# Performance work log

Measured on AMD Instinct MI355X. Metric: run time of the kernel, lower is better.

The kernel has to match this reference:

```python
import jax, jax.numpy as jnp
import numpy as np
import math

B, N, L = 1, 256, 384
D_MSA, D_PAIR, H, DH = 256, 128, 8, 32
EPS = 1e-5


def layernorm(x, g, b):
    mu = jnp.mean(x, axis=-1, keepdims=True)
    var = jnp.mean(jnp.square(x - mu), axis=-1, keepdims=True)
    return (x - mu) * jax.lax.rsqrt(var + EPS) * g + b


def setup_inputs() -> dict:
    key = jax.random.key(0)
    ks = jax.random.split(key, 16)
    s_msa = 1.0 / math.sqrt(D_MSA)
    s_pair = 1.0 / math.sqrt(D_PAIR)
    s_hd = 1.0 / math.sqrt(H * DH)
    return {
        "msa": jax.random.normal(ks[0], (B, N, L, D_MSA), jnp.float32),
        "pair": jax.random.normal(ks[1], (B, L, L, D_PAIR), jnp.float32),
        "ln_msa_g": jnp.ones((D_MSA,), jnp.float32),
        "ln_msa_b": jnp.zeros((D_MSA,), jnp.float32),
        "ln_pair_g": jnp.ones((D_PAIR,), jnp.float32),
        "ln_pair_b": jnp.zeros((D_PAIR,), jnp.float32),
        # SequenceWeight projections (stored as (in, out): y = x @ W + b)
        "Wq_sw": jax.random.normal(ks[2], (D_MSA, H * DH), jnp.float32) * s_msa,
        "bq_sw": jnp.zeros((H * DH,), jnp.float32),
        "Wk_sw": jax.random.normal(ks[3], (D_MSA, H * DH), jnp.float32) * s_msa,
        "bk_sw": jnp.zeros((H * DH,), jnp.float32),
        # Main attention projections (bias-free q/k/v)
        "Wq": jax.random.normal(ks[4], (D_MSA, H * DH), jnp.float32) * s_msa,
        "Wk": jax.random.normal(ks[5], (D_MSA, H * DH), jnp.float32) * s_msa,
        "Wv": jax.random.normal(ks[6], (D_MSA, H * DH), jnp.float32) * s_msa,
        "Wb": jax.random.normal(ks[7], (D_PAIR, H), jnp.float32) * s_pair,
        "Wg": jax.random.normal(ks[8], (D_MSA, H * DH), jnp.float32) * s_msa,
        "bg": jnp.ones((H * DH,), jnp.float32),
        "Wo": jax.random.normal(ks[9], (H * DH, D_MSA), jnp.float32) * s_hd,
        "bo": jnp.zeros((D_MSA,), jnp.float32),
    }


def reference(msa, pair, ln_msa_g, ln_msa_b, ln_pair_g, ln_pair_b,
              Wq_sw, bq_sw, Wk_sw, bk_sw, Wq, Wk, Wv, Wb, Wg, bg, Wo, bo):
    b, n, l, _ = msa.shape
    scale = 1.0 / math.sqrt(DH)

    m = layernorm(msa, ln_msa_g, ln_msa_b)  # (B,N,L,d_msa)

    # --- SequenceWeight: per-sequence, per-position, per-head weights ---
    q_sw = (m[:, 0] @ Wq_sw + bq_sw).reshape(b, l, H, DH) * scale   # (B,L,h,d)
    k_sw = (m @ Wk_sw + bk_sw).reshape(b, n, l, H, DH)              # (B,N,L,h,d)
    sw_logits = jnp.einsum('bihd,bnihd->bnih', q_sw, k_sw)
    seq_weight = jax.nn.softmax(sw_logits, axis=1)[..., None]       # (B,N,L,h,1)

    # --- Row attention with pair bias ---
    q = (m @ Wq).reshape(b, n, l, H, DH) * seq_weight               # seq-weighted queries
    k = (m @ Wk).reshape(b, n, l, H, DH) * scale
    logits = jnp.einsum('bnihd,bnjhd->bijh', q, k)                  # sum over N and d
    bias = layernorm(pair, ln_pair_g, ln_pair_b) @ Wb               # (B,L,L,h)
    attn = jax.nn.softmax(logits + bias, axis=2)                    # softmax over j

    v = (m @ Wv).reshape(b, n, l, H, DH)
    out = jnp.einsum('bijh,bnjhd->bnihd', attn, v).reshape(b, n, l, H * DH)

    gate = jax.nn.sigmoid(m @ Wg + bg)
    return (out * gate) @ Wo + bo                                   # (B,N,L,d_msa)
```

## Files before the change

kernel.cpp:

```cpp
#include <hip/hip_runtime.h>
#include <stdint.h>

#define NSEQ 256
#define LRES 384
#define NH   8
#define NL   (NSEQ*LRES)
#define SCALE 0.17677669529663687f

typedef unsigned short u16;
typedef unsigned int   u32;
typedef short bf16x8 __attribute__((ext_vector_type(8)));
typedef float f32x4  __attribute__((ext_vector_type(4)));

__device__ __forceinline__ u16 f2bf(float f) {
    u32 x = __float_as_uint(f);
    return (u16)((x + 0x7fffu + ((x >> 16) & 1u)) >> 16);
}
__device__ __forceinline__ u32 pack2(float a, float b) {
    u32 xa = __float_as_uint(a);
    u32 xb = __float_as_uint(b);
    xa = (xa + 0x7fffu + ((xa >> 16) & 1u)) >> 16;
    xb = ((xb + 0x7fffu + ((xb >> 16) & 1u)) >> 16) << 16;
    return xa | xb;
}
__device__ __forceinline__ uint4 pack8(const float f[8]) {
    uint4 r;
    r.x = pack2(f[0], f[1]); r.y = pack2(f[2], f[3]);
    r.z = pack2(f[4], f[5]); r.w = pack2(f[6], f[7]);
    return r;
}
__device__ __forceinline__ void unpack2(u32 u, float& f0, float& f1) {
    f0 = __uint_as_float((u & 0xffffu) << 16);
    f1 = __uint_as_float(u & 0xffff0000u);
}
__device__ __forceinline__ void unpack8(uint4 p, float f[8]) {
    unpack2(p.x, f[0], f[1]);
    unpack2(p.y, f[2], f[3]);
    unpack2(p.z, f[4], f[5]);
    unpack2(p.w, f[6], f[7]);
}

__device__ __forceinline__ float wred_sum(float v) {
#pragma unroll
    for (int o = 32; o > 0; o >>= 1) v += __shfl_xor(v, o, 64);
    return v;
}
__device__ __forceinline__ float wred_max(float v) {
#pragma unroll
    for (int o = 32; o > 0; o >>= 1) v = fmaxf(v, __shfl_xor(v, o, 64));
    return v;
}

__global__ __launch_bounds__(256) void ln_msa_k(
    const float* __restrict__ x, const float* __restrict__ g,
    const float* __restrict__ b, u16* __restrict__ lnA,
    float* __restrict__ stats)
{
    const int lane = threadIdx.x & 63;
    const int row = blockIdx.x * 4 + (threadIdx.x >> 6);
    const size_t base = (size_t)row * 256 + lane * 4;
    float4 v = *(const float4*)(x + base);
    float s  = wred_sum(v.x + v.y + v.z + v.w);
    float sq = wred_sum(v.x*v.x + v.y*v.y + v.z*v.z + v.w*v.w);
    const float mu  = s * (1.f / 256.f);
    const float var = sq * (1.f / 256.f) - mu * mu;
    const float rs  = rsqrtf(var + 1e-5f);
    if (lane == 0) {
        stats[(size_t)row * 2]     = mu;
        stats[(size_t)row * 2 + 1] = rs;
    }
    float4 gg = *(const float4*)(g + lane * 4);
    float4 bb = *(const float4*)(b + lane * 4);
    float f0 = (v.x - mu) * rs * gg.x + bb.x;
    float f1 = (v.y - mu) * rs * gg.y + bb.y;
    float f2 = (v.z - mu) * rs * gg.z + bb.z;
    float f3 = (v.w - mu) * rs * gg.w + bb.w;
    uint2 pk;
    pk.x = pack2(f0, f1);
    pk.y = pack2(f2, f3);
    *(uint2*)(lnA + base) = pk;
}

__global__ __launch_bounds__(256) void wconv_k(
    const float* __restrict__ W0, const float* __restrict__ W1,
    const float* __restrict__ W2, const float* __restrict__ W3,
    const float* __restrict__ W4, const float* __restrict__ W5,
    u16* __restrict__ outAll)
{
    const float* Wsrc[6] = {W0, W1, W2, W3, W4, W5};
    const int widx = blockIdx.x >> 4;
    const int tile = blockIdx.x & 15;
    const int kt = tile >> 2, ct = tile & 3;
    const float* W = Wsrc[widx];
    __shared__ float ts[64][65];
    const int r  = threadIdx.x >> 2;
    const int cg = threadIdx.x & 3;
#pragma unroll
    for (int jj = 0; jj < 4; ++jj) {
        float4 v = *(const float4*)(W + (size_t)(kt * 64 + r) * 256
                                      + ct * 64 + cg * 16 + jj * 4);
        ts[r][cg * 16 + jj * 4 + 0] = v.x;
        ts[r][cg * 16 + jj * 4 + 1] = v.y;
        ts[r][cg * 16 + jj * 4 + 2] = v.z;
        ts[r][cg * 16 + jj * 4 + 3] = v.w;
    }
    __syncthreads();
    float lo[8], hi[8];
#pragma unroll
    for (int j = 0; j < 8; ++j) lo[j] = ts[cg * 16 + j][r];
#pragma unroll
    for (int j = 0; j < 8; ++j) hi[j] = ts[cg * 16 + 8 + j][r];
    u16* o = outAll + (size_t)widx * 65536 + (size_t)(ct * 64 + r) * 256
           + kt * 64 + cg * 16;
    *(uint4*)(o)     = pack8(lo);
    *(uint4*)(o + 8) = pack8(hi);
}

__global__ __launch_bounds__(128) void wbprep_k(
    const float* __restrict__ g, const float* __restrict__ b,
    const float* __restrict__ Wb, float* __restrict__ Wp,
    float* __restrict__ AB)
{
    __shared__ float ps[128][8];
    __shared__ float pb[128][8];
    const int c = threadIdx.x;
    const float gc = g[c], bc = b[c];
    float4 w0 = *(const float4*)(Wb + (size_t)c * 8);
    float4 w1 = *(const float4*)(Wb + (size_t)c * 8 + 4);
    const float wraw[8] = {w0.x, w0.y, w0.z, w0.w, w1.x, w1.y, w1.z, w1.w};
    float wp[8];
#pragma unroll
    for (int h = 0; h < 8; ++h) {
        wp[h] = wraw[h] * gc;
        ps[c][h] = wp[h];
        pb[c][h] = wraw[h] * bc;
    }
    *(float4*)(Wp + (size_t)c * 8)     = make_float4(wp[0], wp[1], wp[2], wp[3]);
    *(float4*)(Wp + (size_t)c * 8 + 4) = make_float4(wp[4], wp[5], wp[6], wp[7]);
    __syncthreads();
    if (c < 8) {
        float a = 0.f;
        for (int j = 0; j < 128; ++j) a += ps[j][c];
        AB[c] = a;
    } else if (c < 16) {
        const int h = c - 8;
        float a = 0.f;
        for (int j = 0; j < 128; ++j) a += pb[j][h];
        AB[8 + h] = a;
    }
}

enum { MODE_QSW = 1 };

__global__ __launch_bounds__(256) void gemm_ln_k(
    const void* __restrict__ Av, int a_bf16,
    const float* __restrict__ stats,
    const float* __restrict__ lng, const float* __restrict__ lnb,
    const float* __restrict__ W, const float* __restrict__ bias,
    void* __restrict__ out, const float* __restrict__ seqw, int mode)
{
    __shared__ float As_t[32][68];
    __shared__ float Ws[32][132];
    __shared__ float gs[256], bs[256];
    const int tid = threadIdx.x;
    const int bx = blockIdx.y;
    const int by = blockIdx.x;
    const int tx = tid & 15, ty = tid >> 4;
    const int ar = tid >> 2, acg = tid & 3;
    const int wr = tid >> 3, wcg = tid & 7;
    const bool do_ln = (stats != nullptr);

    if (do_ln) { gs[tid] = lng[tid]; bs[tid] = lnb[tid]; }
    __syncthreads();

    const int arow_idx = by * 64 + ar;
    float mu = 0.f, rsg = 0.f;
    if (do_ln) {
        mu  = stats[(size_t)arow_idx * 2];
        rsg = stats[(size_t)arow_idx * 2 + 1];
    }

    float acc[4][8];
#pragma unroll
    for (int i = 0; i < 4; ++i)
#pragma unroll
        for (int j = 0; j < 8; ++j) acc[i][j] = 0.f;

    const size_t arow = (size_t)arow_idx * 256 + acg * 8;

    for (int kk = 0; kk < 256; kk += 32) {
        float af[8];
        if (a_bf16) {
            uint4 a8 = *(const uint4*)((const u16*)Av + arow + kk);
            unpack8(a8, af);
        } else {
            float4 x0 = *(const float4*)((const float*)Av + arow + kk);
            float4 x1 = *(const float4*)((const float*)Av + arow + kk + 4);
            af[0] = x0.x; af[1] = x0.y; af[2] = x0.z; af[3] = x0.w;
            af[4] = x1.x; af[5] = x1.y; af[6] = x1.z; af[7] = x1.w;
        }
        const float* wrow = W + (size_t)(kk + wr) * 256 + bx * 128 + wcg * 16;
        float4 w0 = *(const float4*)(wrow);
        float4 w1 = *(const float4*)(wrow + 4);
        float4 w2 = *(const float4*)(wrow + 8);
        float4 w3 = *(const float4*)(wrow + 12);
        if (do_ln) {
#pragma unroll
            for (int j = 0; j < 8; ++j) {
                const int k = kk + acg * 8 + j;
                af[j] = (af[j] - mu) * rsg * gs[k] + bs[k];
            }
        }
        __syncthreads();
#pragma unroll
        for (int j = 0; j < 8; ++j) As_t[acg * 8 + j][ar] = af[j];
        float* wsrow = &Ws[wr][wcg * 16];
        *(float4*)(wsrow)      = w0;
        *(float4*)(wsrow + 4)  = w1;
        *(float4*)(wsrow + 8)  = w2;
        *(float4*)(wsrow + 12) = w3;
        __syncthreads();
#pragma unroll 8
        for (int k = 0; k < 32; ++k) {
            const float4 a  = *(const float4*)&As_t[k][ty * 4];
            const float4 b0 = *(const float4*)&Ws[k][tx * 8];
            const float4 b1 = *(const float4*)&Ws[k][tx * 8 + 4];
            const float av[4] = {a.x, a.y, a.z, a.w};
            const float bv[8] = {b0.x, b0.y, b0.z, b0.w, b1.x, b1.y, b1.z, b1.w};
#pragma unroll
            for (int i = 0; i < 4; ++i)
#pragma unroll
                for (int j = 0; j < 8; ++j)
                    acc[i][j] = fmaf(av[i], bv[j], acc[i][j]);
        }
    }

    const int gc0 = bx * 128 + tx * 8;
    float bias8[8] = {0.f, 0.f, 0.f, 0.f, 0.f, 0.f, 0.f, 0.f};
    if (bias) {
#pragma unroll
        for (int j = 0; j < 8; ++j) bias8[j] = bias[gc0 + j];
    }

    float* o = (float*)out;
#pragma unroll
    for (int i = 0; i < 4; ++i) {
        const size_t gr = (size_t)by * 64 + ty * 4 + i;
#pragma unroll
        for (int j = 0; j < 8; ++j)
            o[gr * 256 + gc0 + j] = (acc[i][j] + bias8[j]) * SCALE;
    }
}

__global__ __launch_bounds__(256) void swl_dot_k(
    const float* __restrict__ qsw, const u16* __restrict__ ksw,
    float* __restrict__ swl)
{
    const int gid = blockIdx.x * 256 + threadIdx.x;
    const int r = gid >> 3, h = gid & 7;
    const int i = r % LRES;
    const float* qp = qsw + (size_t)i * 256 + h * 32;
    const uint4* kp = (const uint4*)(ksw + (size_t)r * 256 + h * 32);
    float s = 0.f;
#pragma unroll
    for (int g4 = 0; g4 < 4; ++g4) {
        float kf[8]; unpack8(kp[g4], kf);
#pragma unroll
        for (int j = 0; j < 8; ++j) s += qp[g4 * 8 + j] * kf[j];
    }
    swl[gid] = s;
}

__global__ __launch_bounds__(256) void softmax_n_k(float* __restrict__ swl)
{
    const int col = blockIdx.x * 4 + (threadIdx.x >> 6);
    const int lane = threadIdx.x & 63;
    float* base = swl + col;
    float v[4];
#pragma unroll
    for (int t = 0; t < 4; ++t) v[t] = base[(size_t)(lane * 4 + t) * 3072];
    float mx = wred_max(fmaxf(fmaxf(v[0], v[1]), fmaxf(v[2], v[3])));
    float e[4], s = 0.f;
#pragma unroll
    for (int t = 0; t < 4; ++t) { e[t] = __expf(v[t] - mx); s += e[t]; }
    s = wred_sum(s);
    const float inv = 1.f / s;
#pragma unroll
    for (int t = 0; t < 4; ++t) base[(size_t)(lane * 4 + t) * 3072] = e[t] * inv;
}

__global__ __launch_bounds__(256) void pair_bias_k(
    const float* __restrict__ pairX, const float* __restrict__ Wp,
    const float* __restrict__ AB, float* __restrict__ biasH)
{
    __shared__ float ws[128][8];
    __shared__ float As[8], Bs[8];
    const int tid = threadIdx.x;
    {
        float4 w4 = *(const float4*)(Wp + tid * 4);
        *(float4*)(&ws[tid >> 1][(tid & 1) * 4]) = w4;
    }
    if (tid < 8)       As[tid] = AB[tid];
    else if (tid < 16) Bs[tid - 8] = AB[tid];
    __syncthreads();

    const int lane = tid & 63;
    const int p  = lane >> 3;
    const int cg = lane & 7;
    const size_t pb = (size_t)blockIdx.x * 32 + (tid >> 6) * 8 + p;
    const float* src = pairX + pb * 128 + cg * 16;
    float x[16];
    *(float4*)(x)      = *(const float4*)(src);
    *(float4*)(x + 4)  = *(const float4*)(src + 4);
    *(float4*)(x + 8)  = *(const float4*)(src + 8);
    *(float4*)(x + 12) = *(const float4*)(src + 12);

    float s = 0.f, sq = 0.f;
#pragma unroll
    for (int j = 0; j < 16; ++j) { s += x[j]; sq += x[j] * x[j]; }
#pragma unroll
    for (int o = 1; o <= 4; o <<= 1) {
        s  += __shfl_xor(s, o, 64);
        sq += __shfl_xor(sq, o, 64);
    }
    const float mu  = s * (1.f / 128.f);
    const float var = sq * (1.f / 128.f) - mu * mu;
    const float rs  = rsqrtf(var + 1e-5f);

    float acc[8];
#pragma unroll
    for (int hh = 0; hh < 8; ++hh) {
        const int h = hh ^ cg;
        float a = 0.f;
#pragma unroll
        for (int j = 0; j < 16; ++j) a += x[j] * ws[cg * 16 + j][h];
        acc[hh] = a;
    }
#pragma unroll
    for (int o = 1; o <= 4; o <<= 1) {
        float nv[8];
#pragma unroll
        for (int hh = 0; hh < 8; ++hh)
            nv[hh] = acc[hh] + __shfl_xor(acc[hh ^ o], o, 64);
#pragma unroll
        for (int hh = 0; hh < 8; ++hh) acc[hh] = nv[hh];
    }
    const float res = rs * acc[0] - rs * mu * As[cg] + Bs[cg];
    biasH[pb * 8 + cg] = res;
}

__device__ __forceinline__ void stage128x64(
    const u16* __restrict__ src, size_t rowStride, u16* lds, int tid)
{
    const int row   = tid >> 1;
    const int cbase = (tid & 1) * 4;
#pragma unroll
    for (int ch = 0; ch < 4; ++ch) {
        const int cc = cbase + ch;
        const uint4 v = *(const uint4*)(src + (size_t)row * rowStride + cc * 8);
        *(uint4*)(lds + row * 64 + ((cc ^ (row & 7)) * 8)) = v;
    }
}

__device__ __forceinline__ bf16x8 frag_read(const u16* lds, int row, int kchunk)
{
    return *(const bf16x8*)(lds + row * 64 + ((kchunk ^ (row & 7)) * 8));
}

enum { PROJ_KSW = 0, PROJ_QT = 1, PROJ_KT = 2, PROJ_VT = 3,
       PROJ_GATE = 4, PROJ_OUT = 5 };

__global__ __launch_bounds__(256) void proj_mfma(
    const u16* __restrict__ A, const u16* __restrict__ Wt,
    const float* __restrict__ bias, const float* __restrict__ seqw,
    void* __restrict__ out, int mode)
{
    __shared__ u16 tA[128 * 64];
    __shared__ u16 tW[128 * 64];

    int wg = (blockIdx.x & 7) * 192 + (blockIdx.x >> 3);
    const int rowTile = wg >> 1;
    const int colTile = wg & 1;

    const int tid  = threadIdx.x;
    const int lane = tid & 63, wid = tid >> 6;
    const int wr = wid >> 1, wc = wid & 1;
    const int g  = lane >> 4;
    const int mrow = wr * 64 + (lane & 15);
    const int nrow = wc * 64 + (lane & 15);

    f32x4 acc[4][4];
#pragma unroll
    for (int m = 0; m < 4; ++m)
#pragma unroll
        for (int n = 0; n < 4; ++n) {
            f32x4 z = {0.f, 0.f, 0.f, 0.f};
            acc[m][n] = z;
        }

    const u16* Ab = A  + (size_t)rowTile * 128 * 256;
    const u16* Wb = Wt + (size_t)colTile * 128 * 256;

    for (int k0 = 0; k0 < 256; k0 += 64) {
        stage128x64(Ab + k0, 256, tA, tid);
        stage128x64(Wb + k0, 256, tW, tid);
        __syncthreads();
#pragma unroll
        for (int ks = 0; ks < 2; ++ks) {
            bf16x8 wf[4], af[4];
#pragma unroll
            for (int m = 0; m < 4; ++m) wf[m] = frag_read(tW, mrow + m * 16, ks * 4 + g);
#pragma unroll
            for (int n = 0; n < 4; ++n) af[n] = frag_read(tA, nrow + n * 16, ks * 4 + g);
#pragma unroll
            for (int m = 0; m < 4; ++m)
#pragma unroll
                for (int n = 0; n < 4; ++n)
                    acc[m][n] = __builtin_amdgcn_mfma_f32_16x16x32_bf16(
                        wf[m], af[n], acc[m][n], 0, 0, 0);
        }
        __syncthreads();
    }

    const int cq0 = colTile * 128 + wr * 64 + ((lane >> 4) << 2);
    const int r0  = rowTile * 128 + wc * 64 + (lane & 15);

#pragma unroll
    for (int m = 0; m < 4; ++m) {
        const int c = cq0 + m * 16;
#pragma unroll
        for (int n = 0; n < 4; ++n) {
            const int r = r0 + n * 16;
            const f32x4 a = acc[m][n];
            if (mode == PROJ_KSW || mode == PROJ_GATE) {
                float f0 = a[0] + bias[c];
                float f1 = a[1] + bias[c + 1];
                float f2 = a[2] + bias[c + 2];
                float f3 = a[3] + bias[c + 3];
                if (mode == PROJ_GATE) {
                    f0 = 1.f / (1.f + __expf(-f0));
                    f1 = 1.f / (1.f + __expf(-f1));
                    f2 = 1.f / (1.f + __expf(-f2));
                    f3 = 1.f / (1.f + __expf(-f3));
                }
                uint2 pk;
                pk.x = pack2(f0, f1);
                pk.y = pack2(f2, f3);
                *(uint2*)((u16*)out + (size_t)r * 256 + c) = pk;
            } else if (mode == PROJ_QT || mode == PROJ_KT) {
                const int h = c >> 5, d = c & 31;
                const int n_ = r / LRES, ii = r % LRES;
                const float mult = (mode == PROJ_QT)
                    ? seqw[(size_t)r * NH + h] : SCALE;
                uint2 pk;
                pk.x = pack2(a[0] * mult, a[1] * mult);
                pk.y = pack2(a[2] * mult, a[3] * mult);
                *(uint2*)((u16*)out + (size_t)h * 3145728
                          + (size_t)ii * 8192 + n_ * 32 + d) = pk;
            } else if (mode == PROJ_VT) {
                const int h = c >> 5, d = c & 31;
                const int n_ = r / LRES, ii = r % LRES;
                u16* o = (u16*)out + (size_t)h * 3145728
                       + (size_t)(n_ * 32 + d) * 384 + ii;
                o[0]   = f2bf(a[0]);
                o[384] = f2bf(a[1]);
                o[768] = f2bf(a[2]);
                o[1152] = f2bf(a[3]);
            } else {
                float* o = (float*)out + (size_t)r * 256 + c;
                o[0] = a[0] + bias[c];
                o[1] = a[1] + bias[c + 1];
                o[2] = a[2] + bias[c + 2];
                o[3] = a[3] + bias[c + 3];
            }
        }
    }
}

__global__ __launch_bounds__(256) void gemm_logits_mfma(
    const u16* __restrict__ qT, const u16* __restrict__ kT,
    float* __restrict__ part)
{
    __shared__ u16 tQ[128 * 64];
    __shared__ u16 tK[128 * 64];

    int wg = (blockIdx.x & 7) * 36 + (blockIdx.x >> 3);
    const int gsel = wg / 9;
    const int t    = wg % 9;
    const int h  = gsel >> 2, kc = gsel & 3;
    const int bi = t / 3, bj = t % 3;

    const u16* Q = qT + (size_t)h * 3145728 + (size_t)bi * 128 * 8192;
    const u16* K = kT + (size_t)h * 3145728 + (size_t)bj * 128 * 8192;

    const int tid  = threadIdx.x;
    const int lane = tid & 63, wid = tid >> 6;
    const int wr = wid >> 1, wc = wid & 1;
    const int g  = lane >> 4;
    const int mrow = wr * 64 + (lane & 15);
    const int nrow = wc * 64 + (lane & 15);

    f32x4 acc[4][4];
#pragma unroll
    for (int m = 0; m < 4; ++m)
#pragma unroll
        for (int n = 0; n < 4; ++n) {
            f32x4 z = {0.f, 0.f, 0.f, 0.f};
            acc[m][n] = z;
        }

    const int k0beg = kc * 2048, k0end = k0beg + 2048;
    for (int k0 = k0beg; k0 < k0end; k0 += 64) {
        stage128x64(Q + k0, 8192, tQ, tid);
        stage128x64(K + k0, 8192, tK, tid);
        __syncthreads();
#pragma unroll
        for (int ks = 0; ks < 2; ++ks) {
            bf16x8 kf[4], qf[4];
#pragma unroll
            for (int m = 0; m < 4; ++m) kf[m] = frag_read(tK, mrow + m * 16, ks * 4 + g);
#pragma unroll
            for (int n = 0; n < 4; ++n) qf[n] = frag_read(tQ, nrow + n * 16, ks * 4 + g);
#pragma unroll
            for (int m = 0; m < 4; ++m)
#pragma unroll
                for (int n = 0; n < 4; ++n)
                    acc[m][n] = __builtin_amdgcn_mfma_f32_16x16x32_bf16(
                        kf[m], qf[n], acc[m][n], 0, 0, 0);
        }
        __syncthreads();
    }

    float* dst = part + (size_t)kc * 1179648 + (size_t)h * 147456;
    const int gj_base = bj * 128 + wr * 64 + ((lane >> 4) << 2);
    const int gi_base = bi * 128 + wc * 64 + (lane & 15);
#pragma unroll
    for (int m = 0; m < 4; ++m)
#pragma unroll
        for (int n = 0; n < 4; ++n) {
            const int gi = gi_base + n * 16;
            const int gj = gj_base + m * 16;
            *(f32x4*)(dst + (size_t)gi * 384 + gj) = acc[m][n];
        }
}

__global__ __launch_bounds__(256) void softmax_j_k(
    const float* __restrict__ part, const float* __restrict__ biasH,
    u16* __restrict__ attnB)
{
    const int row = blockIdx.x * 4 + (threadIdx.x >> 6);
    const int lane = threadIdx.x & 63;
    const int h = row / LRES, i = row % LRES;
    const float* p = part + (size_t)h * 147456 + (size_t)i * 384;
    const float* bh = biasH + (size_t)i * 3072 + h;
    float v[6];
#pragma unroll
    for (int t = 0; t < 6; ++t) {
        const int j = t * 64 + lane;
        v[t] = p[j] + p[j + 1179648] + p[j + 2359296] + p[j + 3538944]
             + bh[(size_t)j * 8];
    }
    float mx = v[0];
#pragma unroll
    for (int t = 1; t < 6; ++t) mx = fmaxf(mx, v[t]);
    mx = wred_max(mx);
    float e[6], s = 0.f;
#pragma unroll
    for (int t = 0; t < 6; ++t) { e[t] = __expf(v[t] - mx); s += e[t]; }
    s = wred_sum(s);
    const float inv = 1.f / s;
    u16* ab = attnB + (size_t)h * 147456 + (size_t)i * 384;
#pragma unroll
    for (int t = 0; t < 6; ++t) ab[t * 64 + lane] = f2bf(e[t] * inv);
}

__global__ __launch_bounds__(256) void gemm_out_mfma(
    const u16* __restrict__ attnB, const u16* __restrict__ vTT,
    u16* gate_io)
{
    __shared__ u16 tV[128 * 64];
    __shared__ u16 tA[128 * 64];

    int wg = (blockIdx.x & 7) * 192 + (blockIdx.x >> 3);
    const int h  = wg / 192;
    const int r  = wg % 192;
    const int bn = r / 3;
    const int bi = r % 3;

    const u16* A = attnB + (size_t)h * 147456 + (size_t)bi * 128 * 384;
    const u16* V = vTT   + (size_t)h * 3145728 + (size_t)bn * 128 * 384;

    const int tid  = threadIdx.x;
    const int lane = tid & 63, wid = tid >> 6;
    const int wr = wid >> 1, wc = wid & 1;
    const int g  = lane >> 4;
    const int mrow = wr * 64 + (lane & 15);
    const int nrow = wc * 64 + (lane & 15);

    f32x4 acc[4][4];
#pragma unroll
    for (int m = 0; m < 4; ++m)
#pragma unroll
        for (int n = 0; n < 4; ++n) {
            f32x4 z = {0.f, 0.f, 0.f, 0.f};
            acc[m][n] = z;
        }

    for (int j0 = 0; j0 < 384; j0 += 64) {
        stage128x64(V + j0, 384, tV, tid);
        stage128x64(A + j0, 384, tA, tid);
        __syncthreads();
#pragma unroll
        for (int ks = 0; ks < 2; ++ks) {
            bf16x8 vf[4], af[4];
#pragma unroll
            for (int m = 0; m < 4; ++m) vf[m] = frag_read(tV, mrow + m * 16, ks * 4 + g);
#pragma unroll
            for (int n = 0; n < 4; ++n) af[n] = frag_read(tA, nrow + n * 16, ks * 4 + g);
#pragma unroll
            for (int m = 0; m < 4; ++m)
#pragma unroll
                for (int n = 0; n < 4; ++n)
                    acc[m][n] = __builtin_amdgcn_mfma_f32_16x16x32_bf16(
                        vf[m], af[n], acc[m][n], 0, 0, 0);
        }
        __syncthreads();
    }

    const int nd_base = bn * 128 + wr * 64 + ((lane >> 4) << 2);
    const int i_base  = bi * 128 + wc * 64 + (lane & 15);
#pragma unroll
    for (int m = 0; m < 4; ++m) {
        const int nd = nd_base + m * 16;
        const int nseq = nd >> 5, d = nd & 31;
#pragma unroll
        for (int n = 0; n < 4; ++n) {
            const int gi = i_base + n * 16;
            const size_t addr = ((size_t)(nseq * LRES + gi)) * 256 + h * 32 + d;
            uint2 g2 = *(const uint2*)(gate_io + addr);
            float gf[4];
            unpack2(g2.x, gf[0], gf[1]);
            unpack2(g2.y, gf[2], gf[3]);
            const f32x4 a = acc[m][n];
            uint2 pk;
            pk.x = pack2(a[0] * gf[0], a[1] * gf[1]);
            pk.y = pack2(a[2] * gf[2], a[3] * gf[3]);
            *(uint2*)(gate_io + addr) = pk;
        }
    }
}

extern "C" void kernel_launch(void* const* d_in, const int* in_sizes, int n_in,
                              void* d_out, int out_size, void* d_ws, size_t ws_size,
                              hipStream_t stream)
{
    const float* msa       = (const float*)d_in[0];
    const float* pair      = (const float*)d_in[1];
    const float* ln_msa_g  = (const float*)d_in[2];
    const float* ln_msa_b  = (const float*)d_in[3];
    const float* ln_pair_g = (const float*)d_in[4];
    const float* ln_pair_b = (const float*)d_in[5];
    const float* Wq_sw     = (const float*)d_in[6];
    const float* bq_sw     = (const float*)d_in[7];
    const float* Wk_sw     = (const float*)d_in[8];
    const float* bk_sw     = (const float*)d_in[9];
    const float* Wq        = (const float*)d_in[10];
    const float* Wk        = (const float*)d_in[11];
    const float* Wv        = (const float*)d_in[12];
    const float* Wb        = (const float*)d_in[13];
    const float* Wg        = (const float*)d_in[14];
    const float* bg        = (const float*)d_in[15];
    const float* Wo        = (const float*)d_in[16];
    const float* bo        = (const float*)d_in[17];
    float* out = (float*)d_out;

    char* ws = (char*)d_ws;
    u16*   slotA  = (u16*)(ws + 0);
    u16*   slotB  = (u16*)(ws + 50331648);
    float* stats  = (float*)(ws + 100663296);
    float* qsw    = (float*)(ws + 101449728);
    float* swl    = (float*)(ws + 101842944);
    float* biasH  = (float*)(ws + 104988672);
    float* part   = (float*)(ws + 109707264);
    u16*   attnB  = (u16*)(ws + 128581632);
    u16*   lnA    = (u16*)(ws + 130940928);
    u16*   WtAll  = (u16*)(ws + 181272576);
    float* Wp     = (float*)(ws + 182059008);
    float* AB     = (float*)(ws + 182063104);

    u16* Wt_ksw = WtAll;
    u16* Wt_q   = WtAll + 65536;
    u16* Wt_k   = WtAll + 131072;
    u16* Wt_v   = WtAll + 196608;
    u16* Wt_g   = WtAll + 262144;
    u16* Wt_o   = WtAll + 327680;

    ln_msa_k<<<NL / 4, 256, 0, stream>>>(msa, ln_msa_g, ln_msa_b, lnA, stats);
    wconv_k<<<96, 256, 0, stream>>>(Wk_sw, Wq, Wk, Wv, Wg, Wo, WtAll);
    wbprep_k<<<1, 128, 0, stream>>>(ln_pair_g, ln_pair_b, Wb, Wp, AB);
    proj_mfma<<<1536, 256, 0, stream>>>(lnA, Wt_ksw, bk_sw, nullptr, slotA, PROJ_KSW);
    gemm_ln_k<<<dim3(LRES / 64, 2), 256, 0, stream>>>(
        msa, 0, stats, ln_msa_g, ln_msa_b, Wq_sw, bq_sw, qsw, nullptr, MODE_QSW);
    swl_dot_k<<<NL * NH / 256, 256, 0, stream>>>(qsw, slotA, swl);
    softmax_n_k<<<LRES * NH / 4, 256, 0, stream>>>(swl);
    proj_mfma<<<1536, 256, 0, stream>>>(lnA, Wt_q, nullptr, swl, slotA, PROJ_QT);
    proj_mfma<<<1536, 256, 0, stream>>>(lnA, Wt_k, nullptr, nullptr, slotB, PROJ_KT);
    pair_bias_k<<<LRES * LRES / 32, 256, 0, stream>>>(pair, Wp, AB, biasH);
    gemm_logits_mfma<<<288, 256, 0, stream>>>(slotA, slotB, part);
    softmax_j_k<<<NH * LRES / 4, 256, 0, stream>>>(part, biasH, attnB);
    proj_mfma<<<1536, 256, 0, stream>>>(lnA, Wt_v, nullptr, nullptr, slotA, PROJ_VT);
    proj_mfma<<<1536, 256, 0, stream>>>(lnA, Wt_g, bg, nullptr, slotB, PROJ_GATE);
    gemm_out_mfma<<<1536, 256, 0, stream>>>(attnB, slotA, slotB);
    proj_mfma<<<1536, 256, 0, stream>>>(slotB, Wt_o, bo, nullptr, out, PROJ_OUT);
}
```

Baseline: 640.2 us.

## Fuse K_sw, K, V and gate projections into one kernel with swl dot epilogue

Merges four separate projection launches (K_sw, K, V, gate) into a single kernel that reuses the same A row tile, running four GEMMs back to back per block. The K_sw projection is no longer written to memory. Its epilogue directly computes the sequence-weight logits against q_sw with a cross-lane shuffle reduction, which removes the swl_dot_k kernel and the bf16 K_sw round trip. The workspace is re-laid out with more buffers so K, V and gate can coexist, which needs a larger workspace and makes each block run longer.

```diff
diff --git a/kernel.cpp b/kernel.cpp
--- a/kernel.cpp
+++ b/kernel.cpp
@@ -149,8 +149,6 @@
         AB[8 + h] = a;
     }
 }
-
-enum { MODE_QSW = 1 };
 
 __global__ __launch_bounds__(256) void gemm_ln_k(
     const void* __restrict__ Av, int a_bf16,
@@ -236,11 +234,9 @@
     }
 
     const int gc0 = bx * 128 + tx * 8;
-    float bias8[8] = {0.f, 0.f, 0.f, 0.f, 0.f, 0.f, 0.f, 0.f};
-    if (bias) {
-#pragma unroll
-        for (int j = 0; j < 8; ++j) bias8[j] = bias[gc0 + j];
-    }
+    float bias8[8];
+#pragma unroll
+    for (int j = 0; j < 8; ++j) bias8[j] = bias[gc0 + j];
 
     float* o = (float*)out;
 #pragma unroll
@@ -250,25 +246,6 @@
         for (int j = 0; j < 8; ++j)
             o[gr * 256 + gc0 + j] = (acc[i][j] + bias8[j]) * SCALE;
     }
-}
-
-__global__ __launch_bounds__(256) void swl_dot_k(
-    const float* __restrict__ qsw, const u16* __restrict__ ksw,
-    float* __restrict__ swl)
-{
-    const int gid = blockIdx.x * 256 + threadIdx.x;
-    const int r = gid >> 3, h = gid & 7;
-    const int i = r % LRES;
-    const float* qp = qsw + (size_t)i * 256 + h * 32;
-    const uint4* kp = (const uint4*)(ksw + (size_t)r * 256 + h * 32);
-    float s = 0.f;
-#pragma unroll
-    for (int g4 = 0; g4 < 4; ++g4) {
-        float kf[8]; unpack8(kp[g4], kf);
-#pragma unroll
-        for (int j = 0; j < 8; ++j) s += qp[g4 * 8 + j] * kf[j];
-    }
-    swl[gid] = s;
 }
 
 __global__ __launch_bounds__(256) void softmax_n_k(float* __restrict__ swl)
@@ -367,13 +344,47 @@
     return *(const bf16x8*)(lds + row * 64 + ((kchunk ^ (row & 7)) * 8));
 }
 
-enum { PROJ_KSW = 0, PROJ_QT = 1, PROJ_KT = 2, PROJ_VT = 3,
-       PROJ_GATE = 4, PROJ_OUT = 5 };
-
-__global__ __launch_bounds__(256) void proj_mfma(
-    const u16* __restrict__ A, const u16* __restrict__ Wt,
-    const float* __restrict__ bias, const float* __restrict__ seqw,
-    void* __restrict__ out, int mode)
+__device__ __forceinline__ void proj_core(
+    const u16* __restrict__ Ab, const u16* __restrict__ Wb,
+    u16* tA, u16* tW, int tid, int mrow, int nrow, int g, f32x4 acc[4][4])
+{
+#pragma unroll
+    for (int m = 0; m < 4; ++m)
+#pragma unroll
+        for (int n = 0; n < 4; ++n) {
+            f32x4 z = {0.f, 0.f, 0.f, 0.f};
+            acc[m][n] = z;
+        }
+    for (int k0 = 0; k0 < 256; k0 += 64) {
+        stage128x64(Ab + k0, 256, tA, tid);
+        stage128x64(Wb + k0, 256, tW, tid);
+        __syncthreads();
+#pragma unroll
+        for (int ks = 0; ks < 2; ++ks) {
+            bf16x8 wf[4], af[4];
+#pragma unroll
+            for (int m = 0; m < 4; ++m) wf[m] = frag_read(tW, mrow + m * 16, ks * 4 + g);
+#pragma unroll
+            for (int n = 0; n < 4; ++n) af[n] = frag_read(tA, nrow + n * 16, ks * 4 + g);
+#pragma unroll
+            for (int m = 0; m < 4; ++m)
+#pragma unroll
+                for (int n = 0; n < 4; ++n)
+                    acc[m][n] = __builtin_amdgcn_mfma_f32_16x16x32_bf16(
+                        wf[m], af[n], acc[m][n], 0, 0, 0);
+        }
+        __syncthreads();
+    }
+}
+
+__global__ __launch_bounds__(256) void proj4_mfma(
+    const u16* __restrict__ A,
+    const u16* __restrict__ Wt_ksw, const u16* __restrict__ Wt_k,
+    const u16* __restrict__ Wt_v,   const u16* __restrict__ Wt_g,
+    const float* __restrict__ bias_ksw, const float* __restrict__ bias_g,
+    const float* __restrict__ qsw,
+    float* __restrict__ swl, u16* __restrict__ outKT,
+    u16* __restrict__ outVT, u16* __restrict__ outGATE)
 {
     __shared__ u16 tA[128 * 64];
     __shared__ u16 tW[128 * 64];
@@ -389,83 +400,143 @@
     const int mrow = wr * 64 + (lane & 15);
     const int nrow = wc * 64 + (lane & 15);
 
-    f32x4 acc[4][4];
-#pragma unroll
-    for (int m = 0; m < 4; ++m)
-#pragma unroll
-        for (int n = 0; n < 4; ++n) {
-            f32x4 z = {0.f, 0.f, 0.f, 0.f};
-            acc[m][n] = z;
-        }
-
-    const u16* Ab = A  + (size_t)rowTile * 128 * 256;
-    const u16* Wb = Wt + (size_t)colTile * 128 * 256;
-
-    for (int k0 = 0; k0 < 256; k0 += 64) {
-        stage128x64(Ab + k0, 256, tA, tid);
-        stage128x64(Wb + k0, 256, tW, tid);
-        __syncthreads();
-#pragma unroll
-        for (int ks = 0; ks < 2; ++ks) {
-            bf16x8 wf[4], af[4];
-#pragma unroll
-            for (int m = 0; m < 4; ++m) wf[m] = frag_read(tW, mrow + m * 16, ks * 4 + g);
-#pragma unroll
-            for (int n = 0; n < 4; ++n) af[n] = frag_read(tA, nrow + n * 16, ks * 4 + g);
-#pragma unroll
-            for (int m = 0; m < 4; ++m)
-#pragma unroll
-                for (int n = 0; n < 4; ++n)
-                    acc[m][n] = __builtin_amdgcn_mfma_f32_16x16x32_bf16(
-                        wf[m], af[n], acc[m][n], 0, 0, 0);
-        }
-        __syncthreads();
-    }
+    const u16* Ab = A + (size_t)rowTile * 128 * 256;
+    const size_t woff = (size_t)colTile * 128 * 256;
 
     const int cq0 = colTile * 128 + wr * 64 + ((lane >> 4) << 2);
     const int r0  = rowTile * 128 + wc * 64 + (lane & 15);
 
+    f32x4 acc[4][4];
+
+    proj_core(Ab, Wt_ksw + woff, tA, tW, tid, mrow, nrow, g, acc);
+    {
+        const int hbase = (colTile * 128 + wr * 64) >> 5;
+#pragma unroll
+        for (int n = 0; n < 4; ++n) {
+            const int r = r0 + n * 16;
+            const int ii = r % LRES;
+            float s0 = 0.f, s1 = 0.f;
+#pragma unroll
+            for (int m = 0; m < 4; ++m) {
+                const int c = cq0 + m * 16;
+                const float4 b4 = *(const float4*)(bias_ksw + c);
+                const float4 q4 = *(const float4*)(qsw + (size_t)ii * 256 + c);
+                const f32x4 a = acc[m][n];
+                const float part = (a[0] + b4.x) * q4.x + (a[1] + b4.y) * q4.y
+                                 + (a[2] + b4.z) * q4.z + (a[3] + b4.w) * q4.w;
+                if (m < 2) s0 += part; else s1 += part;
+            }
+            s0 += __shfl_xor(s0, 16, 64); s0 += __shfl_xor(s0, 32, 64);
+            s1 += __shfl_xor(s1, 16, 64); s1 += __shfl_xor(s1, 32, 64);
+            if (lane < 16) {
+                swl[(size_t)r * 8 + hbase]     = s0;
+                swl[(size_t)r * 8 + hbase + 1] = s1;
+            }
+        }
+    }
+
+    proj_core(Ab, Wt_k + woff, tA, tW, tid, mrow, nrow, g, acc);
 #pragma unroll
     for (int m = 0; m < 4; ++m) {
         const int c = cq0 + m * 16;
+        const int h = c >> 5, d = c & 31;
+#pragma unroll
+        for (int n = 0; n < 4; ++n) {
+            const int r = r0 + n * 16;
+            const int n_ = r / LRES, ii = r % LRES;
+            const f32x4 a = acc[m][n];
+            uint2 pk;
+            pk.x = pack2(a[0] * SCALE, a[1] * SCALE);
+            pk.y = pack2(a[2] * SCALE, a[3] * SCALE);
+            *(uint2*)(outKT + (size_t)h * 3145728
+                      + (size_t)ii * 8192 + n_ * 32 + d) = pk;
+        }
+    }
+
+    proj_core(Ab, Wt_v + woff, tA, tW, tid, mrow, nrow, g, acc);
+#pragma unroll
+    for (int m = 0; m < 4; ++m) {
+        const int c = cq0 + m * 16;
+        const int h = c >> 5, d = c & 31;
+#pragma unroll
+        for (int n = 0; n < 4; ++n) {
+            const int r = r0 + n * 16;
+            const int n_ = r / LRES, ii = r % LRES;
+            const f32x4 a = acc[m][n];
+            u16* o = outVT + (size_t)h * 3145728
+                   + (size_t)(n_ * 32 + d) * 384 + ii;
+            o[0]    = f2bf(a[0]);
+            o[384]  = f2bf(a[1]);
+            o[768]  = f2bf(a[2]);
+            o[1152] = f2bf(a[3]);
+        }
+    }
+
+    proj_core(Ab, Wt_g + woff, tA, tW, tid, mrow, nrow, g, acc);
+#pragma unroll
+    for (int m = 0; m < 4; ++m) {
+        const int c = cq0 + m * 16;
+        const float4 b4 = *(const float4*)(bias_g + c);
 #pragma unroll
         for (int n = 0; n < 4; ++n) {
             const int r = r0 + n * 16;
             const f32x4 a = acc[m][n];
-            if (mode == PROJ_KSW || mode == PROJ_GATE) {
-                float f0 = a[0] + bias[c];
-                float f1 = a[1] + bias[c + 1];
-                float f2 = a[2] + bias[c + 2];
-                float f3 = a[3] + bias[c + 3];
-                if (mode == PROJ_GATE) {
-                    f0 = 1.f / (1.f + __expf(-f0));
-                    f1 = 1.f / (1.f + __expf(-f1));
-                    f2 = 1.f / (1.f + __expf(-f2));
-                    f3 = 1.f / (1.f + __expf(-f3));
-                }
-                uint2 pk;
-                pk.x = pack2(f0, f1);
-                pk.y = pack2(f2, f3);
-                *(uint2*)((u16*)out + (size_t)r * 256 + c) = pk;
-            } else if (mode == PROJ_QT || mode == PROJ_KT) {
+            const float f0 = 1.f / (1.f + __expf(-(a[0] + b4.x)));
+            const float f1 = 1.f / (1.f + __expf(-(a[1] + b4.y)));
+            const float f2 = 1.f / (1.f + __expf(-(a[2] + b4.z)));
+            const float f3 = 1.f / (1.f + __expf(-(a[3] + b4.w)));
+            uint2 pk;
+            pk.x = pack2(f0, f1);
+            pk.y = pack2(f2, f3);
+            *(uint2*)(outGATE + (size_t)r * 256 + c) = pk;
+        }
+    }
+}
+
+enum { PROJ_QT = 1, PROJ_OUT = 5 };
+
+__global__ __launch_bounds__(256) void proj_mfma(
+    const u16* __restrict__ A, const u16* __restrict__ Wt,
+    const float* __restrict__ bias, const float* __restrict__ seqw,
+    void* __restrict__ out, int mode)
+{
+    __shared__ u16 tA[128 * 64];
+    __shared__ u16 tW[128 * 64];
+
+    int wg = (blockIdx.x & 7) * 192 + (blockIdx.x >> 3);
+    const int rowTile = wg >> 1;
+    const int colTile = wg & 1;
+
+    const int tid  = threadIdx.x;
+    const int lane = tid & 63, wid = tid >> 6;
+    const int wr = wid >> 1, wc = wid & 1;
+    const int g  = lane >> 4;
+    const int mrow = wr * 64 + (lane & 15);
+    const int nrow = wc * 64 + (lane & 15);
+
+    f32x4 acc[4][4];
+    proj_core(A + (size_t)rowTile * 128 * 256, Wt + (size_t)colTile * 128 * 256,
+              tA, tW, tid, mrow, nrow, g, acc);
+
+    const int cq0 = colTile * 128 + wr * 64 + ((lane >> 4) << 2);
+    const int r0  = rowTile * 128 + wc * 64 + (lane & 15);
+
+#pragma unroll
+    for (int m = 0; m < 4; ++m) {
+        const int c = cq0 + m * 16;
+#pragma unroll
+        for (int n = 0; n < 4; ++n) {
+            const int r = r0 + n * 16;
+            const f32x4 a = acc[m][n];
+            if (mode == PROJ_QT) {
                 const int h = c >> 5, d = c & 31;
                 const int n_ = r / LRES, ii = r % LRES;
-                const float mult = (mode == PROJ_QT)
-                    ? seqw[(size_t)r * NH + h] : SCALE;
+                const float mult = seqw[(size_t)r * NH + h];
                 uint2 pk;
                 pk.x = pack2(a[0] * mult, a[1] * mult);
                 pk.y = pack2(a[2] * mult, a[3] * mult);
                 *(uint2*)((u16*)out + (size_t)h * 3145728
                           + (size_t)ii * 8192 + n_ * 32 + d) = pk;
-            } else if (mode == PROJ_VT) {
-                const int h = c >> 5, d = c & 31;
-                const int n_ = r / LRES, ii = r % LRES;
-                u16* o = (u16*)out + (size_t)h * 3145728
-                       + (size_t)(n_ * 32 + d) * 384 + ii;
-                o[0]   = f2bf(a[0]);
-                o[384] = f2bf(a[1]);
-                o[768] = f2bf(a[2]);
-                o[1152] = f2bf(a[3]);
             } else {
                 float* o = (float*)out + (size_t)r * 256 + c;
                 o[0] = a[0] + bias[c];
@@ -675,18 +746,20 @@
     float* out = (float*)d_out;
 
     char* ws = (char*)d_ws;
-    u16*   slotA  = (u16*)(ws + 0);
-    u16*   slotB  = (u16*)(ws + 50331648);
-    float* stats  = (float*)(ws + 100663296);
-    float* qsw    = (float*)(ws + 101449728);
-    float* swl    = (float*)(ws + 101842944);
-    float* biasH  = (float*)(ws + 104988672);
-    float* part   = (float*)(ws + 109707264);
-    u16*   attnB  = (u16*)(ws + 128581632);
-    u16*   lnA    = (u16*)(ws + 130940928);
-    u16*   WtAll  = (u16*)(ws + 181272576);
-    float* Wp     = (float*)(ws + 182059008);
-    float* AB     = (float*)(ws + 182063104);
+    u16*   B0 = (u16*)(ws + 0);
+    u16*   B1 = (u16*)(ws + 50331648);
+    u16*   B2 = (u16*)(ws + 100663296);
+    u16*   B3 = (u16*)(ws + 150994944);
+    u16*   lnA = (u16*)(ws + 201326592);
+    float* part  = (float*)(ws + 201326592);
+    u16*   attnB = (u16*)(ws + 201326592 + 18874368);
+    float* biasH = (float*)(ws + 201326592 + 21233664);
+    float* stats = (float*)(ws + 251658240);
+    float* qsw   = (float*)(ws + 252444672);
+    float* swl   = (float*)(ws + 252837888);
+    u16*   WtAll = (u16*)(ws + 255983616);
+    float* Wp    = (float*)(ws + 256770048);
+    float* AB    = (float*)(ws + 256774144);
 
     u16* Wt_ksw = WtAll;
     u16* Wt_q   = WtAll + 65536;
@@ -698,18 +771,15 @@
     ln_msa_k<<<NL / 4, 256, 0, stream>>>(msa, ln_msa_g, ln_msa_b, lnA, stats);
     wconv_k<<<96, 256, 0, stream>>>(Wk_sw, Wq, Wk, Wv, Wg, Wo, WtAll);
     wbprep_k<<<1, 128, 0, stream>>>(ln_pair_g, ln_pair_b, Wb, Wp, AB);
-    proj_mfma<<<1536, 256, 0, stream>>>(lnA, Wt_ksw, bk_sw, nullptr, slotA, PROJ_KSW);
     gemm_ln_k<<<dim3(LRES / 64, 2), 256, 0, stream>>>(
-        msa, 0, stats, ln_msa_g, ln_msa_b, Wq_sw, bq_sw, qsw, nullptr, MODE_QSW);
-    swl_dot_k<<<NL * NH / 256, 256, 0, stream>>>(qsw, slotA, swl);
+        msa, 0, stats, ln_msa_g, ln_msa_b, Wq_sw, bq_sw, qsw, nullptr, 1);
+    proj4_mfma<<<1536, 256, 0, stream>>>(
+        lnA, Wt_ksw, Wt_k, Wt_v, Wt_g, bk_sw, bg, qsw, swl, B1, B2, B3);
     softmax_n_k<<<LRES * NH / 4, 256, 0, stream>>>(swl);
-    proj_mfma<<<1536, 256, 0, stream>>>(lnA, Wt_q, nullptr, swl, slotA, PROJ_QT);
-    proj_mfma<<<1536, 256, 0, stream>>>(lnA, Wt_k, nullptr, nullptr, slotB, PROJ_KT);
+    proj_mfma<<<1536, 256, 0, stream>>>(lnA, Wt_q, nullptr, swl, B0, PROJ_QT);
     pair_bias_k<<<LRES * LRES / 32, 256, 0, stream>>>(pair, Wp, AB, biasH);
-    gemm_logits_mfma<<<288, 256, 0, stream>>>(slotA, slotB, part);
+    gemm_logits_mfma<<<288, 256, 0, stream>>>(B0, B1, part);
     softmax_j_k<<<NH * LRES / 4, 256, 0, stream>>>(part, biasH, attnB);
-    proj_mfma<<<1536, 256, 0, stream>>>(lnA, Wt_v, nullptr, nullptr, slotA, PROJ_VT);
-    proj_mfma<<<1536, 256, 0, stream>>>(lnA, Wt_g, bg, nullptr, slotB, PROJ_GATE);
-    gemm_out_mfma<<<1536, 256, 0, stream>>>(attnB, slotA, slotB);
-    proj_mfma<<<1536, 256, 0, stream>>>(slotB, Wt_o, bo, nullptr, out, PROJ_OUT);
-}
+    gemm_out_mfma<<<1536, 256, 0, stream>>>(attnB, B2, B3);
+    proj_mfma<<<1536, 256, 0, stream>>>(B3, Wt_o, bo, nullptr, out, PROJ_OUT);
+}
```

After: 662.9 us. +3.5%, slower.
